# Performance work log

Hardware: AMD Instinct MI355X
Metric: run time of the kernel (lower is better)

The kernel has to match this reference:

```python
import jax, jax.numpy as jnp
import numpy as np

N = 50000      # nodes
E = 400000     # edges (avg degree 8)
F_IN = 128     # input feature dim
H = 4          # heads (layer 1)
D = 128        # hidden per head
C = 3          # classes (layer 2 out, 1 head)
EPS = 1e-5     # BatchNorm eps
SLOPE = 0.2    # LeakyReLU negative slope (DGL GATConv default)


def setup_inputs() -> dict:
    key = jax.random.key(0)
    ks = jax.random.split(key, 16)
    s = jnp.float32(0.05)
    return {
        "features": jax.random.normal(ks[0], (N, F_IN), jnp.float32),
        "src": jax.random.randint(ks[1], (E,), 0, N, jnp.int32),
        "dst": jax.random.randint(ks[2], (E,), 0, N, jnp.int32),
        # GATConv layer 1 params
        "W1": jax.random.normal(ks[3], (F_IN, H * D), jnp.float32) * s,
        "al1": jax.random.normal(ks[4], (H, D), jnp.float32) * s,
        "ar1": jax.random.normal(ks[5], (H, D), jnp.float32) * s,
        "b1": jnp.zeros((H * D,), jnp.float32),
        "Wres1": jax.random.normal(ks[6], (F_IN, H * D), jnp.float32) * s,
        # BatchNorm1d (inference mode)
        "bn_gamma": jnp.ones((H * D,), jnp.float32),
        "bn_beta": jnp.zeros((H * D,), jnp.float32),
        "bn_mean": jnp.zeros((H * D,), jnp.float32),
        "bn_var": jnp.ones((H * D,), jnp.float32),
        # GATConv layer 2 params (1 head, C out)
        "W2": jax.random.normal(ks[7], (H * D, C), jnp.float32) * s,
        "al2": jax.random.normal(ks[8], (1, C), jnp.float32) * s,
        "ar2": jax.random.normal(ks[9], (1, C), jnp.float32) * s,
        "b2": jnp.zeros((C,), jnp.float32),
        "Wres2": jax.random.normal(ks[10], (H * D, C), jnp.float32) * s,
    }


def _gat_layer(x, src, dst, W, attn_l, attn_r, bias, Wres, heads, dim):
    """DGL GATConv (eval mode): gather, LeakyReLU score, segment softmax,
    weighted scatter-sum, linear residual, bias."""
    n = x.shape[0]
    z = (x @ W).reshape(n, heads, dim)                 # [N,H,D]
    el = jnp.sum(z * attn_l, axis=-1)                  # [N,H]
    er = jnp.sum(z * attn_r, axis=-1)                  # [N,H]
    e = jax.nn.leaky_relu(el[src] + er[dst], SLOPE)    # [E,H]
    # segment softmax over incoming edges of each dst node
    m = jax.ops.segment_max(e, dst, num_segments=n)    # [N,H]
    ex = jnp.exp(e - m[dst])                           # [E,H]
    den = jax.ops.segment_sum(ex, dst, num_segments=n) # [N,H]
    alpha = ex / den[dst]                              # [E,H]
    # weighted message aggregation
    rst = jax.ops.segment_sum(z[src] * alpha[..., None], dst, num_segments=n)  # [N,H,D]
    res = (x @ Wres).reshape(n, heads, dim)
    return rst + res + bias.reshape(1, heads, dim)


def reference(features, src, dst, W1, al1, ar1, b1, Wres1,
              bn_gamma, bn_beta, bn_mean, bn_var,
              W2, al2, ar2, b2, Wres2):
    h = _gat_layer(features, src, dst, W1, al1, ar1, b1, Wres1, H, D)
    h = h.reshape(N, H * D)
    # BatchNorm1d (inference) + ELU; dropout is identity in eval mode
    h = (h - bn_mean) * jax.lax.rsqrt(bn_var + EPS) * bn_gamma + bn_beta
    h = jax.nn.elu(h)
    h = _gat_layer(h, src, dst, W2, al2, ar2, b2, Wres2, 1, C)
    return h[:, 0, :]  # squeeze head dim -> [N, C]
```

## Files before the change

### kernel.cpp

```cpp
#include <hip/hip_runtime.h>
#include <hip/hip_bf16.h>

#define N_NODES 50000
#define N_EDGES 400000
#define FIN     128
#define HD      512
#define SLOPE   0.2f

typedef __hip_bfloat16 bf16;
typedef __bf16 bf16x8 __attribute__((ext_vector_type(8)));
typedef __bf16 bf16x4 __attribute__((ext_vector_type(4)));
typedef __bf16 bf16x2 __attribute__((ext_vector_type(2)));
typedef float  f32x4  __attribute__((ext_vector_type(4)));
typedef float  f32x2  __attribute__((ext_vector_type(2)));

__global__ void sentinel_k(float* out, int n) {
    int i = blockIdx.x * 256 + threadIdx.x;
    if (i < n) out[i] = 12288.0f;
}

__global__ __launch_bounds__(256) void prep_k(const float* __restrict__ W1, const float* __restrict__ Wres1,
                                              const float* __restrict__ al1, const float* __restrict__ ar1,
                                              const float* __restrict__ W2, const float* __restrict__ Wres2,
                                              const float* __restrict__ b1,
                                              const float* __restrict__ bnm, const float* __restrict__ bnv,
                                              const float* __restrict__ bng, const float* __restrict__ bnb,
                                              bf16* __restrict__ Wfrag, float* __restrict__ tab,
                                              float* __restrict__ wl, float* __restrict__ wr,
                                              int* __restrict__ deg) {
    int b = blockIdx.x;
    if (b < 196) {
        int i = b * 256 + threadIdx.x;
        if (i < N_NODES) deg[i] = 0;
        return;
    }
    b -= 196;
    if (b < 64) {
        int f = b * 256 + threadIdx.x;
        int lane = f & 63, unit = f >> 6;
        int tile = unit >> 3, ks = unit & 7;
        int cl = lane & 15, rg = lane >> 4;
        int gc = tile * 16 + cl;
        int k0 = ks * 32 + rg * 8;
        bf16x8 v;
#pragma unroll
        for (int j = 0; j < 8; ++j) {
            int kk = k0 + j;
            float x = (kk < 128) ? W1[kk * HD + gc] : Wres1[(kk - 128) * HD + gc];
            v[j] = (__bf16)x;
        }
        *reinterpret_cast<bf16x8*>(reinterpret_cast<char*>(Wfrag) + (size_t)f * 16) = v;
        return;
    }
    b -= 64;
    if (b < 16) {
        int i = b * 256 + threadIdx.x;
        int gc = i >> 3, c = i & 7;
        float v;
        if (c < 2) {
            float rs = rsqrtf(bnv[gc] + 1e-5f) * bng[gc];
            v = (c == 0) ? rs : (b1[gc] - bnm[gc]) * rs + bnb[gc];
        } else if (c < 5) {
            v = W2[gc * 3 + (c - 2)];
        } else {
            v = Wres2[gc * 3 + (c - 5)];
        }
        tab[i] = v;
        return;
    }
    b -= 16;
    int i = b * 256 + threadIdx.x;
    int k = i >> 2, h = i & 3;
    float sl = 0.f, sr = 0.f;
    for (int d = 0; d < 128; ++d) {
        float w = W1[k * HD + h * 128 + d];
        sl += w * al1[h * 128 + d];
        sr += w * ar1[h * 128 + d];
    }
    wl[k * 4 + h] = sl;
    wr[k * 4 + h] = sr;
}

__global__ __launch_bounds__(256) void eler_k(const float* __restrict__ X,
                                              const float* __restrict__ wl, const float* __restrict__ wr,
                                              float* __restrict__ el, float* __restrict__ er,
                                              bf16* __restrict__ Xb,
                                              const int* __restrict__ dst, int* __restrict__ deg) {
    if (blockIdx.x >= N_NODES / 4) {
        int e = (blockIdx.x - N_NODES / 4) * 256 + threadIdx.x;
        if (e < N_EDGES) atomicAdd(&deg[dst[e]], 1);
        return;
    }
    int w = threadIdx.x >> 6, lane = threadIdx.x & 63;
    int n = blockIdx.x * 4 + w;
    float x1 = X[(size_t)n * FIN + lane];
    float x2 = X[(size_t)n * FIN + 64 + lane];
    Xb[(size_t)n * FIN + lane] = __float2bfloat16(x1);
    Xb[(size_t)n * FIN + 64 + lane] = __float2bfloat16(x2);
    float pl[4], pr[4];
#pragma unroll
    for (int h = 0; h < 4; ++h) {
        pl[h] = x1 * wl[lane * 4 + h] + x2 * wl[(lane + 64) * 4 + h];
        pr[h] = x1 * wr[lane * 4 + h] + x2 * wr[(lane + 64) * 4 + h];
    }
#pragma unroll
    for (int off = 32; off > 0; off >>= 1) {
#pragma unroll
        for (int h = 0; h < 4; ++h) {
            pl[h] += __shfl_xor(pl[h], off);
            pr[h] += __shfl_xor(pr[h], off);
        }
    }
    if (lane == 0) {
        *reinterpret_cast<float4*>(el + (size_t)n * 4) = make_float4(pl[0], pl[1], pl[2], pl[3]);
        *reinterpret_cast<float4*>(er + (size_t)n * 4) = make_float4(pr[0], pr[1], pr[2], pr[3]);
    }
}

__global__ __launch_bounds__(256) void scan1_k(const int* __restrict__ deg,
                                               int* __restrict__ rowptr, int* __restrict__ blksum) {
    __shared__ int wsum[4];
    int t = threadIdx.x, b = blockIdx.x;
    int i = b * 256 + t;
    int v = (i < N_NODES) ? deg[i] : 0;
    int lane = t & 63, w = t >> 6;
    int x = v;
#pragma unroll
    for (int off = 1; off < 64; off <<= 1) {
        int y = __shfl_up(x, off);
        if (lane >= off) x += y;
    }
    if (lane == 63) wsum[w] = x;
    __syncthreads();
    int wadd = 0;
    if (w > 0) wadd += wsum[0];
    if (w > 1) wadd += wsum[1];
    if (w > 2) wadd += wsum[2];
    int incl = x + wadd;
    if (i < N_NODES) rowptr[i] = incl - v;
    if (t == 255) blksum[b] = incl;
}

__global__ __launch_bounds__(256) void scan2_k(int* __restrict__ blksum) {
    __shared__ int wsum[4];
    int t = threadIdx.x;
    int v = (t < 196) ? blksum[t] : 0;
    int lane = t & 63, w = t >> 6;
    int x = v;
#pragma unroll
    for (int off = 1; off < 64; off <<= 1) {
        int y = __shfl_up(x, off);
        if (lane >= off) x += y;
    }
    if (lane == 63) wsum[w] = x;
    __syncthreads();
    int wadd = 0;
    if (w > 0) wadd += wsum[0];
    if (w > 1) wadd += wsum[1];
    if (w > 2) wadd += wsum[2];
    if (t < 196) blksum[t] = x + wadd - v;
}

__global__ __launch_bounds__(256) void scan3_k(const int* __restrict__ blksum,
                                               int* __restrict__ rowptr, int* __restrict__ cursor) {
    int b = blockIdx.x;
    int i = b * 256 + threadIdx.x;
    if (i < N_NODES) {
        int v = rowptr[i] + blksum[b];
        rowptr[i] = v;
        cursor[i] = v;
    }
    if (i == 0) rowptr[N_NODES] = N_EDGES;
}

__global__ void fill_k(const int* __restrict__ src, const int* __restrict__ dst,
                       int* __restrict__ cursor, int* __restrict__ csr) {
    int e = blockIdx.x * 256 + threadIdx.x;
    if (e < N_EDGES) {
        int pos = atomicAdd(&cursor[dst[e]], 1);
        csr[pos] = src[e];
    }
}

__global__ __launch_bounds__(1024) void aggX_k(const int* __restrict__ rowptr, const int* __restrict__ csr,
                                               const float* __restrict__ el, const float* __restrict__ er,
                                               const bf16* __restrict__ Xb, bf16* __restrict__ AGGb) {
    __shared__ int    ssrc[16][64];
    __shared__ float4 spe4[16][64];

    const int w = threadIdx.x >> 6, lane = threadIdx.x & 63;
    const int n = blockIdx.x * 16 + w;
    const int beg = rowptr[n];
    const int deg = rowptr[n + 1] - beg;
    const float4 ern = *reinterpret_cast<const float4*>(er + (size_t)n * 4);
    const char* Xbc = reinterpret_cast<const char*>(Xb);

    f32x2 acc[4] = {{0.f,0.f},{0.f,0.f},{0.f,0.f},{0.f,0.f}};
    float4 den = make_float4(0.f, 0.f, 0.f, 0.f);

    for (int base = 0; base < deg; base += 64) {
        const int cnt = min(64, deg - base);
        if (lane < cnt) {
            int s = csr[beg + base + lane];
            ssrc[w][lane] = s;
            float4 e4 = *reinterpret_cast<const float4*>(el + (size_t)s * 4);
            float4 p; float e;
            e = e4.x + ern.x; e = e > 0.f ? e : SLOPE * e; p.x = __expf(e);
            e = e4.y + ern.y; e = e > 0.f ? e : SLOPE * e; p.y = __expf(e);
            e = e4.z + ern.z; e = e > 0.f ? e : SLOPE * e; p.z = __expf(e);
            e = e4.w + ern.w; e = e > 0.f ? e : SLOPE * e; p.w = __expf(e);
            den.x += p.x; den.y += p.y; den.z += p.z; den.w += p.w;
            spe4[w][lane] = p;
        }
        asm volatile("s_waitcnt lgkmcnt(0)" ::: "memory");
        for (int jj = 0; jj < cnt; jj += 4) {
            unsigned xv[4]; float4 pk[4];
#pragma unroll
            for (int k2 = 0; k2 < 4; ++k2) {
                int j2 = jj + k2;
                int jc = j2 < cnt ? j2 : cnt - 1;
                int s = ssrc[w][jc];
                xv[k2] = *reinterpret_cast<const unsigned*>(Xbc + (size_t)s * 256 + lane * 4);
                float4 p = spe4[w][jc];
                if (j2 >= cnt) p = make_float4(0.f, 0.f, 0.f, 0.f);
                pk[k2] = p;
            }
#pragma unroll
            for (int k2 = 0; k2 < 4; ++k2) {
                f32x2 x2 = {__uint_as_float(xv[k2] << 16), __uint_as_float(xv[k2] & 0xffff0000u)};
                acc[0] += pk[k2].x * x2;
                acc[1] += pk[k2].y * x2;
                acc[2] += pk[k2].z * x2;
                acc[3] += pk[k2].w * x2;
            }
        }
        asm volatile("s_waitcnt lgkmcnt(0)" ::: "memory");
    }

#pragma unroll
    for (int off = 32; off > 0; off >>= 1) {
        den.x += __shfl_xor(den.x, off);
        den.y += __shfl_xor(den.y, off);
        den.z += __shfl_xor(den.z, off);
        den.w += __shfl_xor(den.w, off);
    }
    float inv[4] = {0.f, 0.f, 0.f, 0.f};
    if (deg > 0) {
        inv[0] = 1.f / den.x; inv[1] = 1.f / den.y;
        inv[2] = 1.f / den.z; inv[3] = 1.f / den.w;
    }
#pragma unroll
    for (int h = 0; h < 4; ++h) {
        bf16x2 v = {(__bf16)(acc[h][0] * inv[h]), (__bf16)(acc[h][1] * inv[h])};
        *reinterpret_cast<bf16x2*>(AGGb + (size_t)n * 512 + h * 128 + lane * 2) = v;
    }
}

__global__ __launch_bounds__(256) void gemm2_k(
    const bf16* __restrict__ Xb, const bf16* __restrict__ AGGb,
    const bf16* __restrict__ Wfrag, const float* __restrict__ tab,
    const float* __restrict__ al2, const float* __restrict__ ar2,
    float* __restrict__ node2) {
    __shared__ __align__(16) char XS[32 * 256];
    __shared__ __align__(16) char AGS[32 * 1024];
    __shared__ float zsum[4][32][6];

    const int t = threadIdx.x;
    const int w = t >> 6, lane = t & 63;
    const int cl = lane & 15, rg = lane >> 4;
    const int m0 = blockIdx.x * 32;

#pragma unroll
    for (int j = 0; j < 2; ++j) {
        int L = j * 4096 + t * 16;
        int row = L >> 8, col = L & 255;
        int grow = m0 + row; grow = grow < N_NODES ? grow : N_NODES - 1;
        bf16x8 v = *reinterpret_cast<const bf16x8*>(
            reinterpret_cast<const char*>(Xb) + (size_t)grow * 256 + col);
        int byte = (row * 256 + col) ^ ((row & 7) << 4);
        *reinterpret_cast<bf16x8*>(XS + byte) = v;
    }
#pragma unroll
    for (int j = 0; j < 8; ++j) {
        int L = j * 4096 + t * 16;
        int row = L >> 10, col = L & 1023;
        int grow = m0 + row; grow = grow < N_NODES ? grow : N_NODES - 1;
        bf16x8 v = *reinterpret_cast<const bf16x8*>(
            reinterpret_cast<const char*>(AGGb) + (size_t)grow * 1024 + col);
        int byte = (row * 1024 + col) ^ ((row & 7) << 4);
        *reinterpret_cast<bf16x8*>(AGS + byte) = v;
    }
    __syncthreads();

    float z2p[2][3] = {}, r2p[2][3] = {};

#pragma unroll
    for (int ct = 0; ct < 8; ++ct) {
        const int unit = (w * 8 + ct) * 8;
        bf16x8 af[8];
#pragma unroll
        for (int ks = 0; ks < 8; ++ks)
            af[ks] = *reinterpret_cast<const bf16x8*>(
                reinterpret_cast<const char*>(Wfrag) + ((size_t)(unit + ks) * 64 + lane) * 16);
        const int gcl = w * 128 + ct * 16 + rg * 4;
        f32x4 t0[4], t1[4];
#pragma unroll
        for (int i = 0; i < 4; ++i) {
            t0[i] = *reinterpret_cast<const f32x4*>(tab + (size_t)(gcl + i) * 8);
            t1[i] = *reinterpret_cast<const f32x4*>(tab + (size_t)(gcl + i) * 8 + 4);
        }
#pragma unroll
        for (int mt = 0; mt < 2; ++mt) {
            int row = mt * 16 + cl;
            int swz = (row & 7) << 4;
            f32x4 a = {0.f, 0.f, 0.f, 0.f};
#pragma unroll
            for (int ks = 0; ks < 4; ++ks) {
                int byte = (row * 1024 + w * 256 + ks * 64 + rg * 16) ^ swz;
                bf16x8 bfr = *reinterpret_cast<const bf16x8*>(AGS + byte);
                a = __builtin_amdgcn_mfma_f32_16x16x32_bf16(af[ks], bfr, a, 0, 0, 0);
            }
#pragma unroll
            for (int ks = 0; ks < 4; ++ks) {
                int byte = (row * 256 + ks * 64 + rg * 16) ^ swz;
                bf16x8 bfr = *reinterpret_cast<const bf16x8*>(XS + byte);
                a = __builtin_amdgcn_mfma_f32_16x16x32_bf16(af[ks + 4], bfr, a, 0, 0, 0);
            }
#pragma unroll
            for (int i = 0; i < 4; ++i) {
                float hv = a[i] * t0[i][0] + t0[i][1];
                hv = hv > 0.f ? hv : (__expf(hv) - 1.f);
                z2p[mt][0] += hv * t0[i][2]; z2p[mt][1] += hv * t0[i][3]; z2p[mt][2] += hv * t1[i][0];
                r2p[mt][0] += hv * t1[i][1]; r2p[mt][1] += hv * t1[i][2]; r2p[mt][2] += hv * t1[i][3];
            }
        }
    }

#pragma unroll
    for (int mt = 0; mt < 2; ++mt)
#pragma unroll
        for (int c = 0; c < 3; ++c) {
            z2p[mt][c] += __shfl_xor(z2p[mt][c], 16);
            z2p[mt][c] += __shfl_xor(z2p[mt][c], 32);
            r2p[mt][c] += __shfl_xor(r2p[mt][c], 16);
            r2p[mt][c] += __shfl_xor(r2p[mt][c], 32);
        }
    if (rg == 0) {
#pragma unroll
        for (int mt = 0; mt < 2; ++mt) {
            int nl = mt * 16 + cl;
            zsum[w][nl][0] = z2p[mt][0]; zsum[w][nl][1] = z2p[mt][1]; zsum[w][nl][2] = z2p[mt][2];
            zsum[w][nl][3] = r2p[mt][0]; zsum[w][nl][4] = r2p[mt][1]; zsum[w][nl][5] = r2p[mt][2];
        }
    }
    __syncthreads();
    if (t < 32) {
        float v[6];
#pragma unroll
        for (int c = 0; c < 6; ++c)
            v[c] = zsum[0][t][c] + zsum[1][t][c] + zsum[2][t][c] + zsum[3][t][c];
        int n = m0 + t;
        if (n < N_NODES) {
            float e2l = v[0] * al2[0] + v[1] * al2[1] + v[2] * al2[2];
            float e2r = v[0] * ar2[0] + v[1] * ar2[1] + v[2] * ar2[2];
            *reinterpret_cast<float4*>(node2 + (size_t)n * 8) = make_float4(v[0], v[1], v[2], e2l);
            *reinterpret_cast<float4*>(node2 + (size_t)n * 8 + 4) = make_float4(v[3], v[4], v[5], e2r);
        }
    }
}

__global__ __launch_bounds__(256) void agg2_k(const int* __restrict__ rowptr, const int* __restrict__ csr,
                                              const float* __restrict__ node2,
                                              const float* __restrict__ b2, float* __restrict__ out) {
    int wv = threadIdx.x >> 6, lane = threadIdx.x & 63;
    int n = blockIdx.x * 4 + wv;
    int beg = rowptr[n], deg = rowptr[n + 1] - beg;
    float ern = node2[(size_t)n * 8 + 7];
    float den = 0.f, a0 = 0.f, a1 = 0.f, a2 = 0.f;
    for (int j = lane; j < deg; j += 64) {
        int s = csr[beg + j];
        float4 v = *reinterpret_cast<const float4*>(node2 + (size_t)s * 8);
        float e = v.w + ern;
        e = e > 0.f ? e : SLOPE * e;
        float p = __expf(e);
        den += p;
        a0 += p * v.x; a1 += p * v.y; a2 += p * v.z;
    }
#pragma unroll
    for (int off = 32; off > 0; off >>= 1) {
        den += __shfl_xor(den, off);
        a0 += __shfl_xor(a0, off); a1 += __shfl_xor(a1, off); a2 += __shfl_xor(a2, off);
    }
    if (lane == 0) {
        float inv = deg > 0 ? 1.f / den : 0.f;
        float4 r = *reinterpret_cast<const float4*>(node2 + (size_t)n * 8 + 4);
        out[(size_t)n * 3 + 0] = a0 * inv + r.x + b2[0];
        out[(size_t)n * 3 + 1] = a1 * inv + r.y + b2[1];
        out[(size_t)n * 3 + 2] = a2 * inv + r.z + b2[2];
    }
}

extern "C" void kernel_launch(void* const* d_in, const int* in_sizes, int n_in,
                              void* d_out, int out_size, void* d_ws, size_t ws_size,
                              hipStream_t stream) {
    const float* X     = (const float*)d_in[0];
    const int*   src   = (const int*)d_in[1];
    const int*   dst   = (const int*)d_in[2];
    const float* W1    = (const float*)d_in[3];
    const float* al1   = (const float*)d_in[4];
    const float* ar1   = (const float*)d_in[5];
    const float* b1    = (const float*)d_in[6];
    const float* Wres1 = (const float*)d_in[7];
    const float* bng   = (const float*)d_in[8];
    const float* bnb   = (const float*)d_in[9];
    const float* bnm   = (const float*)d_in[10];
    const float* bnv   = (const float*)d_in[11];
    const float* W2    = (const float*)d_in[12];
    const float* al2   = (const float*)d_in[13];
    const float* ar2   = (const float*)d_in[14];
    const float* b2    = (const float*)d_in[15];
    const float* Wres2 = (const float*)d_in[16];
    float* out = (float*)d_out;

    char* p = (char*)d_ws;
    auto carve = [&](size_t bytes) -> char* {
        char* r = p;
        p += (bytes + 255) & ~(size_t)255;
        return r;
    };
    bf16*  Wfrag  = (bf16*)carve((size_t)512 * 256 * 2);
    float* tab    = (float*)carve((size_t)512 * 8 * 4);
    float* wl     = (float*)carve((size_t)FIN * 4 * 4);
    float* wr     = (float*)carve((size_t)FIN * 4 * 4);
    float* el     = (float*)carve((size_t)N_NODES * 4 * 4);
    float* er     = (float*)carve((size_t)N_NODES * 4 * 4);
    int*   deg    = (int*)carve((size_t)N_NODES * 4);
    int*   rowptr = (int*)carve((size_t)(N_NODES + 1) * 4);
    int*   cursor = (int*)carve((size_t)N_NODES * 4);
    int*   blksum = (int*)carve((size_t)256 * 4);
    int*   csr    = (int*)carve((size_t)N_EDGES * 4);
    bf16*  Xb     = (bf16*)carve((size_t)N_NODES * FIN * 2);
    bf16*  AGGb   = (bf16*)carve((size_t)N_NODES * 512 * 2);
    float* node2  = (float*)carve((size_t)N_NODES * 8 * 4);
    size_t need = (size_t)(p - (char*)d_ws);
    if (need > ws_size) {
        sentinel_k<<<(out_size + 255) / 256, 256, 0, stream>>>(out, out_size);
        return;
    }

    prep_k<<<196 + 64 + 16 + 2, 256, 0, stream>>>(W1, Wres1, al1, ar1, W2, Wres2, b1,
                                                  bnm, bnv, bng, bnb, Wfrag, tab, wl, wr, deg);
    eler_k<<<N_NODES / 4 + (N_EDGES + 255) / 256, 256, 0, stream>>>(X, wl, wr, el, er, Xb, dst, deg);
    scan1_k<<<196, 256, 0, stream>>>(deg, rowptr, blksum);
    scan2_k<<<1, 256, 0, stream>>>(blksum);
    scan3_k<<<196, 256, 0, stream>>>(blksum, rowptr, cursor);
    fill_k<<<(N_EDGES + 255) / 256, 256, 0, stream>>>(src, dst, cursor, csr);
    aggX_k<<<N_NODES / 16, 1024, 0, stream>>>(rowptr, csr, el, er, Xb, AGGb);
    gemm2_k<<<(N_NODES + 31) / 32, 256, 0, stream>>>(Xb, AGGb, Wfrag, tab, al2, ar2, node2);
    agg2_k<<<N_NODES / 4, 256, 0, stream>>>(rowptr, csr, node2, b2, out);
}
```

Baseline: 174.1 us.

## Compute el/er projections with bf16 MFMA over 64-node tiles in eler_k

The per-node attention logit projection, previously one wavefront per node with shuffle reductions, now runs on MFMA 16x16x32 bf16 instructions. Each block stages 64 rows of X as bf16 in swizzled shared memory, using vectorized loads that also write Xb. The projected attention weights are precomputed in prep_k as a bf16 fragment layout. This cuts launched blocks and reduction overhead, at the cost of computing the el/er logits with bf16 inputs and weights, which loses some precision.

Result: slower. 180.4 us (+3.6%).

```diff
diff --git a/kernel.cpp b/kernel.cpp
--- a/kernel.cpp
+++ b/kernel.cpp
@@ -6,6 +6,7 @@
 #define FIN     128
 #define HD      512
 #define SLOPE   0.2f
+#define NB_X    782
 
 typedef __hip_bfloat16 bf16;
 typedef __bf16 bf16x8 __attribute__((ext_vector_type(8)));
@@ -26,7 +27,7 @@
                                               const float* __restrict__ bnm, const float* __restrict__ bnv,
                                               const float* __restrict__ bng, const float* __restrict__ bnb,
                                               bf16* __restrict__ Wfrag, float* __restrict__ tab,
-                                              float* __restrict__ wl, float* __restrict__ wr,
+                                              bf16* __restrict__ wlrb,
                                               int* __restrict__ deg) {
     int b = blockIdx.x;
     if (b < 196) {
@@ -68,52 +69,68 @@
         tab[i] = v;
         return;
     }
-    b -= 16;
-    int i = b * 256 + threadIdx.x;
-    int k = i >> 2, h = i & 3;
-    float sl = 0.f, sr = 0.f;
-    for (int d = 0; d < 128; ++d) {
-        float w = W1[k * HD + h * 128 + d];
-        sl += w * al1[h * 128 + d];
-        sr += w * ar1[h * 128 + d];
-    }
-    wl[k * 4 + h] = sl;
-    wr[k * 4 + h] = sr;
+    for (int i = 0; i < 8; ++i) {
+        int e = i * 256 + threadIdx.x;
+        int ks = e >> 9, lane = (e >> 3) & 63, j = e & 7;
+        int r = lane & 15, rg = lane >> 4;
+        int k = ks * 32 + rg * 8 + j;
+        float v = 0.f;
+        if (r < 4) {
+            for (int d = 0; d < 128; ++d) v += W1[k * HD + r * 128 + d] * al1[r * 128 + d];
+        } else if (r < 8) {
+            int h = r - 4;
+            for (int d = 0; d < 128; ++d) v += W1[k * HD + h * 128 + d] * ar1[h * 128 + d];
+        }
+        wlrb[e] = __float2bfloat16(v);
+    }
 }
 
 __global__ __launch_bounds__(256) void eler_k(const float* __restrict__ X,
-                                              const float* __restrict__ wl, const float* __restrict__ wr,
+                                              const bf16* __restrict__ wlrb,
                                               float* __restrict__ el, float* __restrict__ er,
                                               bf16* __restrict__ Xb,
                                               const int* __restrict__ dst, int* __restrict__ deg) {
-    if (blockIdx.x >= N_NODES / 4) {
-        int e = (blockIdx.x - N_NODES / 4) * 256 + threadIdx.x;
+    if (blockIdx.x >= NB_X) {
+        int e = (blockIdx.x - NB_X) * 256 + threadIdx.x;
         if (e < N_EDGES) atomicAdd(&deg[dst[e]], 1);
         return;
     }
-    int w = threadIdx.x >> 6, lane = threadIdx.x & 63;
-    int n = blockIdx.x * 4 + w;
-    float x1 = X[(size_t)n * FIN + lane];
-    float x2 = X[(size_t)n * FIN + 64 + lane];
-    Xb[(size_t)n * FIN + lane] = __float2bfloat16(x1);
-    Xb[(size_t)n * FIN + 64 + lane] = __float2bfloat16(x2);
-    float pl[4], pr[4];
-#pragma unroll
-    for (int h = 0; h < 4; ++h) {
-        pl[h] = x1 * wl[lane * 4 + h] + x2 * wl[(lane + 64) * 4 + h];
-        pr[h] = x1 * wr[lane * 4 + h] + x2 * wr[(lane + 64) * 4 + h];
-    }
-#pragma unroll
-    for (int off = 32; off > 0; off >>= 1) {
-#pragma unroll
-        for (int h = 0; h < 4; ++h) {
-            pl[h] += __shfl_xor(pl[h], off);
-            pr[h] += __shfl_xor(pr[h], off);
-        }
-    }
-    if (lane == 0) {
-        *reinterpret_cast<float4*>(el + (size_t)n * 4) = make_float4(pl[0], pl[1], pl[2], pl[3]);
-        *reinterpret_cast<float4*>(er + (size_t)n * 4) = make_float4(pr[0], pr[1], pr[2], pr[3]);
+    __shared__ __align__(16) char XSb[64 * 256];
+    const int t = threadIdx.x;
+    const int w = t >> 6, lane = t & 63;
+    const int cl = lane & 15, rg = lane >> 4;
+    const int m0 = blockIdx.x * 64;
+
+#pragma unroll
+    for (int j = 0; j < 8; ++j) {
+        int e = j * 1024 + t * 4;
+        int row = e >> 7, col = e & 127;
+        int grow = m0 + row;
+        int gc = grow < N_NODES ? grow : N_NODES - 1;
+        f32x4 v = *reinterpret_cast<const f32x4*>(X + (size_t)gc * FIN + col);
+        bf16x4 bv = {(__bf16)v[0], (__bf16)v[1], (__bf16)v[2], (__bf16)v[3]};
+        if (grow < N_NODES)
+            *reinterpret_cast<bf16x4*>(Xb + (size_t)grow * FIN + col) = bv;
+        int byte = (row * 256 + col * 2) ^ ((row & 7) << 4);
+        *reinterpret_cast<bf16x4*>(XSb + byte) = bv;
+    }
+    __syncthreads();
+
+    f32x4 a = {0.f, 0.f, 0.f, 0.f};
+    const int row = w * 16 + cl;
+    const int swz = (row & 7) << 4;
+#pragma unroll
+    for (int ks = 0; ks < 4; ++ks) {
+        bf16x8 af = *reinterpret_cast<const bf16x8*>(
+            reinterpret_cast<const char*>(wlrb) + ((size_t)(ks * 64 + lane)) * 16);
+        int byte = (row * 256 + ks * 64 + rg * 16) ^ swz;
+        bf16x8 bf = *reinterpret_cast<const bf16x8*>(XSb + byte);
+        a = __builtin_amdgcn_mfma_f32_16x16x32_bf16(af, bf, a, 0, 0, 0);
+    }
+    int n = m0 + row;
+    if (n < N_NODES) {
+        if (rg == 0)      *reinterpret_cast<float4*>(el + (size_t)n * 4) = make_float4(a[0], a[1], a[2], a[3]);
+        else if (rg == 1) *reinterpret_cast<float4*>(er + (size_t)n * 4) = make_float4(a[0], a[1], a[2], a[3]);
     }
 }
 
@@ -430,8 +447,7 @@
     };
     bf16*  Wfrag  = (bf16*)carve((size_t)512 * 256 * 2);
     float* tab    = (float*)carve((size_t)512 * 8 * 4);
-    float* wl     = (float*)carve((size_t)FIN * 4 * 4);
-    float* wr     = (float*)carve((size_t)FIN * 4 * 4);
+    bf16*  wlrb   = (bf16*)carve((size_t)2048 * 2);
     float* el     = (float*)carve((size_t)N_NODES * 4 * 4);
     float* er     = (float*)carve((size_t)N_NODES * 4 * 4);
     int*   deg    = (int*)carve((size_t)N_NODES * 4);
@@ -448,9 +464,9 @@
         return;
     }
 
-    prep_k<<<196 + 64 + 16 + 2, 256, 0, stream>>>(W1, Wres1, al1, ar1, W2, Wres2, b1,
-                                                  bnm, bnv, bng, bnb, Wfrag, tab, wl, wr, deg);
-    eler_k<<<N_NODES / 4 + (N_EDGES + 255) / 256, 256, 0, stream>>>(X, wl, wr, el, er, Xb, dst, deg);
+    prep_k<<<196 + 64 + 16 + 1, 256, 0, stream>>>(W1, Wres1, al1, ar1, W2, Wres2, b1,
+                                                  bnm, bnv, bng, bnb, Wfrag, tab, wlrb, deg);
+    eler_k<<<NB_X + (N_EDGES + 255) / 256, 256, 0, stream>>>(X, wlrb, el, er, Xb, dst, deg);
     scan1_k<<<196, 256, 0, stream>>>(deg, rowptr, blksum);
     scan2_k<<<1, 256, 0, stream>>>(blksum);
     scan3_k<<<196, 256, 0, stream>>>(blksum, rowptr, cursor);
```
